# Kernel optimization log

Hardware: AMD Instinct MI355X
Metric: run time of the kernel (lower is better)

Reference implementation:

```python
import jax, jax.numpy as jnp
import numpy as np

H, W = 256, 256
N_PIX = H * W
MAX_DIST = float(np.sqrt(H ** 2 + W ** 2))


def _img_locations(dtype):
    # cartesian([arange(H), arange(W)]) -> row-major (h, w) pairs, matches prob_map.reshape(-1)
    hh, ww = jnp.meshgrid(jnp.arange(H), jnp.arange(W), indexing="ij")
    return jnp.stack([hh, ww], axis=-1).reshape(-1, 2).astype(dtype)  # [N, 2]


def setup_inputs() -> dict:
    key = jax.random.key(0)
    k1, k2 = jax.random.split(key)
    prob_map = jax.random.uniform(k1, (4, H, W), dtype=jnp.float32)
    gt_points = jax.random.randint(k2, (4, 512, 2), 0, 256, dtype=jnp.int32)
    return {"prob_map": prob_map, "gt_points": gt_points}


def reference(prob_map, gt_points):
    # prob_map: [B, H, W] float; gt_points: [B, G, 2] int pixel coords.
    # orig_sizes == resized_size in the original module, so norm_factor == 1.
    dtype = prob_map.dtype
    B = prob_map.shape[0]
    locs = _img_locations(dtype)                      # [N, 2]
    gt = gt_points.astype(dtype)                      # [B, G, 2]

    # pairwise euclidean distances via expanded form (avoids [B,N,G,2] tensor)
    x2 = jnp.sum(locs * locs, axis=-1)[None, :, None]       # [1, N, 1]
    y2 = jnp.sum(gt * gt, axis=-1)[:, None, :]              # [B, 1, G]
    xy = jnp.einsum("nd,bgd->bng", locs, gt)                # [B, N, G]
    d = jnp.sqrt(jnp.maximum(x2 + y2 - 2.0 * xy, 0.0))      # [B, N, G]

    p = prob_map.reshape(B, -1)                             # [B, N]
    n_est = jnp.sum(p, axis=-1)                             # [B]

    # term_1: prob-weighted min distance from each pixel to nearest gt point
    term_1 = jnp.sum(p * jnp.min(d, axis=-1), axis=-1) / (n_est + 1e-6)  # [B]

    # term_2: min over pixels of prob-weighted distance, averaged over gt points
    weighted_d = (1.0 - p)[:, :, None] * MAX_DIST + p[:, :, None] * d    # [B, N, G]
    term_2 = jnp.mean(jnp.min(weighted_d, axis=1), axis=-1)             # [B]

    return jnp.mean(term_1) + jnp.mean(term_2)
```

## Files before the change

### kernel.cpp

```cpp
#include <hip/hip_runtime.h>

#define NPIX  65536
#define NG    512
#define NB    4
#define MAXD  362.03867196751236f
#define WRAD  24
#define WDIM  49
#define WCNT  2401
#define SAFE_Q (23.0f - MAXD)
#define NBLK_T1 256
#define NBLK_T2 (NB*NG)
#define NBLK_MAIN (NBLK_T1 + NBLK_T2)
#define BRAD 32
#define BSPAN 68
#define BCAP 320


__device__ __forceinline__ float wave_sum(float v){
  #pragma unroll
  for (int o = 32; o > 0; o >>= 1) v += __shfl_down(v, o, 64);
  return v;
}
__device__ __forceinline__ float wave_min(float v){
  #pragma unroll
  for (int o = 32; o > 0; o >>= 1) v = fminf(v, __shfl_down(v, o, 64));
  return v;
}

__global__ __launch_bounds__(256) void k_main(const float* __restrict__ prob,
                                              const int* __restrict__ gt,
                                              float* __restrict__ wsout){
  const int tid  = threadIdx.x;
  const int lane = tid & 63;
  const int wid  = tid >> 6;

  if (blockIdx.x < NBLK_T1){
    __shared__ float2 bsab[BCAP + 1];
    __shared__ float red[8];
    __shared__ int bcnt, ovf, anybad;
    const int b  = blockIdx.x >> 6;
    const int hp = (blockIdx.x & 63) << 2;
    const float wf = (float)tid;

    if (tid == 0){ bcnt = 0; ovf = 0; anybad = 0; }
    __syncthreads();

    const int2* gtp = ((const int2*)gt) + b*NG;
    #pragma unroll
    for (int s = 0; s < 2; ++s){
      const int g = tid + 256*s;
      const int2 q = gtp[g];
      const bool in = ((unsigned)(q.x - (hp - BRAD)) < (unsigned)BSPAN);
      const unsigned long long mk = __ballot(in);
      int base = 0;
      if (lane == 0) base = atomicAdd(&bcnt, (int)__popcll(mk));
      base = __shfl(base, 0, 64);
      if (in){
        const int pos = base + (int)__popcll(mk & ((1ULL << lane) - 1ULL));
        if (pos < BCAP) bsab[pos] = make_float2(-2.0f*(float)q.x, -2.0f*(float)q.y);
        else ovf = 1;
      }
    }
    __syncthreads();
    const int Lc = min(bcnt, BCAP);
    if (tid == 0) bsab[Lc] = make_float2(-20000.0f, -20000.0f);
    __syncthreads();
    const int pairs = (Lc + 1) >> 1;

    float hf[4], m[4];
    #pragma unroll
    for (int r = 0; r < 4; ++r){ hf[r] = (float)(hp + r); m[r] = 3e38f; }

    #pragma unroll 4
    for (int k = 0; k < pairs; ++k){
      const float2 q0 = bsab[2*k + 0];
      const float2 q1 = bsab[2*k + 1];
      const float sc0 = fmaf(q0.y, q0.y, q0.x*q0.x) * 0.25f;
      const float sc1 = fmaf(q1.y, q1.y, q1.x*q1.x) * 0.25f;
      const float u0  = fmaf(q0.y, wf, sc0);
      const float u1  = fmaf(q1.y, wf, sc1);
      #pragma unroll
      for (int r = 0; r < 4; ++r){
        const float t0 = fmaf(q0.x, hf[r], u0);
        const float t1 = fmaf(q1.x, hf[r], u1);
        m[r] = fminf(fminf(m[r], t0), t1);
      }
    }

    const float w2 = (float)(tid*tid);
    float v[4];
    int bad = ovf;
    #pragma unroll
    for (int r = 0; r < 4; ++r){
      v[r] = m[r] + fmaf(hf[r], hf[r], w2);
      bad |= (v[r] > 1024.0f);
    }
    if (bad) anybad = 1;
    __syncthreads();

    if (anybad){
      #pragma unroll
      for (int r = 0; r < 4; ++r) m[r] = 3e38f;
      for (int g = 0; g < NG; ++g){
        const int2 q = gtp[g];
        const float ax = -2.0f*(float)q.x, ay = -2.0f*(float)q.y;
        const float sc = fmaf(ay, ay, ax*ax) * 0.25f;
        const float u  = fmaf(ay, wf, sc);
        #pragma unroll
        for (int r = 0; r < 4; ++r)
          m[r] = fminf(m[r], fmaf(ax, hf[r], u));
      }
      #pragma unroll
      for (int r = 0; r < 4; ++r) v[r] = m[r] + fmaf(hf[r], hf[r], w2);
    }

    float spd = 0.0f, sp = 0.0f;
    #pragma unroll
    for (int r = 0; r < 4; ++r){
      const float d = __builtin_amdgcn_sqrtf(v[r]);
      const float p = prob[b*NPIX + (hp + r)*256 + tid];
      spd = fmaf(p, d, spd);
      sp += p;
    }

    spd = wave_sum(spd);
    sp  = wave_sum(sp);
    if (lane == 0){ red[wid] = spd; red[4+wid] = sp; }
    __syncthreads();
    if (tid == 0){
      wsout[blockIdx.x]       = (red[0]+red[1]) + (red[2]+red[3]);
      wsout[512 + blockIdx.x] = (red[4]+red[5]) + (red[6]+red[7]);
    }
  } else {
    __shared__ float red[8];
    const int idx = blockIdx.x - NBLK_T1;
    const int b   = idx >> 9;
    const int gh  = gt[idx*2 + 0];
    const int gw  = gt[idx*2 + 1];

    float qm = 3e38f;
    for (int i = tid; i < WCNT; i += 256){
      const int r  = i / WDIM;
      const int c  = i - r*WDIM;
      const int hh = gh - WRAD + r;
      const int ww = gw - WRAD + c;
      if ((unsigned)hh < 256u && (unsigned)ww < 256u){
        const float p  = prob[b*NPIX + hh*256 + ww];
        const int  dh  = r - WRAD, dw = c - WRAD;
        const float d  = __builtin_amdgcn_sqrtf((float)(dh*dh + dw*dw));
        qm = fminf(qm, fmaf(p, d, p * (-MAXD)));
      }
    }
    qm = wave_min(qm);
    if (lane == 0) red[wid] = qm;
    __syncthreads();
    float qf = fminf(fminf(red[0], red[1]), fminf(red[2], red[3]));

    if (qf > SAFE_Q){
      const float ghf = (float)gh, gwf = (float)gw;
      const float aa  = -2.0f*ghf;
      const float wf  = (float)tid;
      const float bc  = fmaf(-2.0f*gwf, wf, fmaf(ghf, ghf, gwf*gwf));
      const float wsq = wf*wf;
      float q2 = 3e38f;
      const float* pr = prob + b*NPIX + tid;
      #pragma unroll 4
      for (int i = 0; i < 256; ++i){
        const float p   = pr[i*256];
        const float hfi = (float)i;
        const float d2v = fmaf(aa, hfi, fmaf(hfi, hfi, wsq) + bc);
        const float d   = __builtin_amdgcn_sqrtf(d2v);
        q2 = fminf(q2, fmaf(p, d, p * (-MAXD)));
      }
      q2 = wave_min(q2);
      __syncthreads();
      if (lane == 0) red[wid] = q2;
      __syncthreads();
      qf = fminf(fminf(red[0], red[1]), fminf(red[2], red[3]));
    }
    if (tid == 0) wsout[1024 + idx] = qf;
  }
}

__global__ __launch_bounds__(256) void k_finish(const float* __restrict__ ws,
                                                float* __restrict__ out){
  const int tid  = threadIdx.x;
  const int w    = tid >> 6;
  const int lane = tid & 63;
  __shared__ float redT2[4];
  __shared__ float t1sh[NB];

  float s = 0.0f;
  #pragma unroll
  for (int j = 0; j < 8; ++j) s += ws[1024 + tid*8 + j];
  s = wave_sum(s);
  if (lane == 0) redT2[w] = s;

  float pd = ws[w*64 + lane];
  float pp = ws[512 + w*64 + lane];
  pd = wave_sum(pd);
  pp = wave_sum(pp);
  if (lane == 0) t1sh[w] = pd / (pp + 1e-6f);
  __syncthreads();

  if (tid == 0){
    const float s2    = (redT2[0]+redT2[1]) + (redT2[2]+redT2[3]);
    const float term2 = MAXD + s2 * (1.0f/2048.0f);
    const float term1 = ((t1sh[0]+t1sh[1]) + (t1sh[2]+t1sh[3])) * 0.25f;
    out[0] = term1 + term2;
  }
}

extern "C" void kernel_launch(void* const* d_in, const int* in_sizes, int n_in,
                              void* d_out, int out_size, void* d_ws, size_t ws_size,
                              hipStream_t stream) {
  const float* prob = (const float*)d_in[0];
  const int*   gt   = (const int*)d_in[1];
  float* out = (float*)d_out;
  float* ws  = (float*)d_ws;

  hipLaunchKernelGGL(k_main,   dim3(NBLK_MAIN), dim3(256), 0, stream, prob, gt, ws);
  hipLaunchKernelGGL(k_finish, dim3(1),         dim3(256), 0, stream, ws, out);
}
```

Before: 15.79 us.

## Fuse finish reduction into main kernel via last-block atomic counter

Merges the two-kernel sequence into one kernel. The last block to finish, found through an atomic counter and threadfence, runs the final reduction. Term-2 blocks now each handle four GT points in sequence, so the grid shrinks from 2304 to 768 blocks. This removes one kernel launch and its dependency gap, but adds a memset, serialises work inside each term-2 block, and adds extra barriers per point.

```diff
diff --git a/kernel.cpp b/kernel.cpp
--- a/kernel.cpp
+++ b/kernel.cpp
@@ -9,12 +9,13 @@
 #define WCNT  2401
 #define SAFE_Q (23.0f - MAXD)
 #define NBLK_T1 256
-#define NBLK_T2 (NB*NG)
-#define NBLK_MAIN (NBLK_T1 + NBLK_T2)
+#define NBLK_T2 512
+#define NBLK    (NBLK_T1 + NBLK_T2)
 #define BRAD 32
 #define BSPAN 68
 #define BCAP 320
 
+#define CNT_OFF 3072
 
 __device__ __forceinline__ float wave_sum(float v){
   #pragma unroll
@@ -27,16 +28,18 @@
   return v;
 }
 
-__global__ __launch_bounds__(256) void k_main(const float* __restrict__ prob,
-                                              const int* __restrict__ gt,
-                                              float* __restrict__ wsout){
+__global__ __launch_bounds__(256) void k_all(const float* __restrict__ prob,
+                                             const int* __restrict__ gt,
+                                             float* __restrict__ ws,
+                                             float* __restrict__ out){
   const int tid  = threadIdx.x;
   const int lane = tid & 63;
   const int wid  = tid >> 6;
+  __shared__ float red[8];
+  __shared__ int   lastFlag;
 
   if (blockIdx.x < NBLK_T1){
     __shared__ float2 bsab[BCAP + 1];
-    __shared__ float red[8];
     __shared__ int bcnt, ovf, anybad;
     const int b  = blockIdx.x >> 6;
     const int hp = (blockIdx.x & 63) << 2;
@@ -128,86 +131,94 @@
     if (lane == 0){ red[wid] = spd; red[4+wid] = sp; }
     __syncthreads();
     if (tid == 0){
-      wsout[blockIdx.x]       = (red[0]+red[1]) + (red[2]+red[3]);
-      wsout[512 + blockIdx.x] = (red[4]+red[5]) + (red[6]+red[7]);
+      ws[blockIdx.x]       = (red[0]+red[1]) + (red[2]+red[3]);
+      ws[512 + blockIdx.x] = (red[4]+red[5]) + (red[6]+red[7]);
     }
   } else {
-    __shared__ float red[8];
-    const int idx = blockIdx.x - NBLK_T1;
-    const int b   = idx >> 9;
-    const int gh  = gt[idx*2 + 0];
-    const int gw  = gt[idx*2 + 1];
-
-    float qm = 3e38f;
-    for (int i = tid; i < WCNT; i += 256){
-      const int r  = i / WDIM;
-      const int c  = i - r*WDIM;
-      const int hh = gh - WRAD + r;
-      const int ww = gw - WRAD + c;
-      if ((unsigned)hh < 256u && (unsigned)ww < 256u){
-        const float p  = prob[b*NPIX + hh*256 + ww];
-        const int  dh  = r - WRAD, dw = c - WRAD;
-        const float d  = __builtin_amdgcn_sqrtf((float)(dh*dh + dw*dw));
-        qm = fminf(qm, fmaf(p, d, p * (-MAXD)));
-      }
-    }
-    qm = wave_min(qm);
-    if (lane == 0) red[wid] = qm;
-    __syncthreads();
-    float qf = fminf(fminf(red[0], red[1]), fminf(red[2], red[3]));
-
-    if (qf > SAFE_Q){
-      const float ghf = (float)gh, gwf = (float)gw;
-      const float aa  = -2.0f*ghf;
-      const float wf  = (float)tid;
-      const float bc  = fmaf(-2.0f*gwf, wf, fmaf(ghf, ghf, gwf*gwf));
-      const float wsq = wf*wf;
-      float q2 = 3e38f;
-      const float* pr = prob + b*NPIX + tid;
-      #pragma unroll 4
-      for (int i = 0; i < 256; ++i){
-        const float p   = pr[i*256];
-        const float hfi = (float)i;
-        const float d2v = fmaf(aa, hfi, fmaf(hfi, hfi, wsq) + bc);
-        const float d   = __builtin_amdgcn_sqrtf(d2v);
-        q2 = fminf(q2, fmaf(p, d, p * (-MAXD)));
-      }
-      q2 = wave_min(q2);
+    const int j2 = blockIdx.x - NBLK_T1;
+    for (int s = 0; s < 4; ++s){
+      const int idx = j2*4 + s;
+      const int b   = idx >> 9;
+      const int gh  = gt[idx*2 + 0];
+      const int gw  = gt[idx*2 + 1];
+
+      float qm = 3e38f;
+      for (int i = tid; i < WCNT; i += 256){
+        const int r  = i / WDIM;
+        const int c  = i - r*WDIM;
+        const int hh = gh - WRAD + r;
+        const int ww = gw - WRAD + c;
+        if ((unsigned)hh < 256u && (unsigned)ww < 256u){
+          const float p  = prob[b*NPIX + hh*256 + ww];
+          const int  dh  = r - WRAD, dw = c - WRAD;
+          const float d  = __builtin_amdgcn_sqrtf((float)(dh*dh + dw*dw));
+          qm = fminf(qm, fmaf(p, d, p * (-MAXD)));
+        }
+      }
+      qm = wave_min(qm);
+      if (lane == 0) red[wid] = qm;
       __syncthreads();
-      if (lane == 0) red[wid] = q2;
+      float qf = fminf(fminf(red[0], red[1]), fminf(red[2], red[3]));
+
+      if (qf > SAFE_Q){
+        const float ghf = (float)gh, gwf = (float)gw;
+        const float aa  = -2.0f*ghf;
+        const float wf  = (float)tid;
+        const float bc  = fmaf(-2.0f*gwf, wf, fmaf(ghf, ghf, gwf*gwf));
+        const float wsq = wf*wf;
+        float q2 = 3e38f;
+        const float* pr = prob + b*NPIX + tid;
+        #pragma unroll 4
+        for (int i = 0; i < 256; ++i){
+          const float p   = pr[i*256];
+          const float hfi = (float)i;
+          const float d2v = fmaf(aa, hfi, fmaf(hfi, hfi, wsq) + bc);
+          const float d   = __builtin_amdgcn_sqrtf(d2v);
+          q2 = fminf(q2, fmaf(p, d, p * (-MAXD)));
+        }
+        q2 = wave_min(q2);
+        __syncthreads();
+        if (lane == 0) red[wid] = q2;
+        __syncthreads();
+        qf = fminf(fminf(red[0], red[1]), fminf(red[2], red[3]));
+      }
+      if (tid == 0) ws[1024 + idx] = qf;
       __syncthreads();
-      qf = fminf(fminf(red[0], red[1]), fminf(red[2], red[3]));
-    }
-    if (tid == 0) wsout[1024 + idx] = qf;
+    }
   }
-}
-
-__global__ __launch_bounds__(256) void k_finish(const float* __restrict__ ws,
-                                                float* __restrict__ out){
-  const int tid  = threadIdx.x;
-  const int w    = tid >> 6;
-  const int lane = tid & 63;
-  __shared__ float redT2[4];
-  __shared__ float t1sh[NB];
-
-  float s = 0.0f;
-  #pragma unroll
-  for (int j = 0; j < 8; ++j) s += ws[1024 + tid*8 + j];
-  s = wave_sum(s);
-  if (lane == 0) redT2[w] = s;
-
-  float pd = ws[w*64 + lane];
-  float pp = ws[512 + w*64 + lane];
-  pd = wave_sum(pd);
-  pp = wave_sum(pp);
-  if (lane == 0) t1sh[w] = pd / (pp + 1e-6f);
+
   __syncthreads();
-
   if (tid == 0){
-    const float s2    = (redT2[0]+redT2[1]) + (redT2[2]+redT2[3]);
-    const float term2 = MAXD + s2 * (1.0f/2048.0f);
-    const float term1 = ((t1sh[0]+t1sh[1]) + (t1sh[2]+t1sh[3])) * 0.25f;
-    out[0] = term1 + term2;
+    __threadfence();
+    const unsigned t = atomicAdd((unsigned*)(ws + CNT_OFF), 1u);
+    lastFlag = (t == NBLK - 1u);
+  }
+  __syncthreads();
+  if (lastFlag){
+    __threadfence();
+    __shared__ float redT2[4];
+    __shared__ float t1sh[NB];
+    const int w = wid;
+
+    float s = 0.0f;
+    #pragma unroll
+    for (int j = 0; j < 8; ++j) s += ws[1024 + tid*8 + j];
+    s = wave_sum(s);
+    if (lane == 0) redT2[w] = s;
+
+    float pd = ws[w*64 + lane];
+    float pp = ws[512 + w*64 + lane];
+    pd = wave_sum(pd);
+    pp = wave_sum(pp);
+    if (lane == 0) t1sh[w] = pd / (pp + 1e-6f);
+    __syncthreads();
+
+    if (tid == 0){
+      const float s2    = (redT2[0]+redT2[1]) + (redT2[2]+redT2[3]);
+      const float term2 = MAXD + s2 * (1.0f/2048.0f);
+      const float term1 = ((t1sh[0]+t1sh[1]) + (t1sh[2]+t1sh[3])) * 0.25f;
+      out[0] = term1 + term2;
+    }
   }
 }
 
@@ -219,6 +230,6 @@
   float* out = (float*)d_out;
   float* ws  = (float*)d_ws;
 
-  hipLaunchKernelGGL(k_main,   dim3(NBLK_MAIN), dim3(256), 0, stream, prob, gt, ws);
-  hipLaunchKernelGGL(k_finish, dim3(1),         dim3(256), 0, stream, ws, out);
-}
+  hipMemsetAsync(ws + CNT_OFF, 0, 4, stream);
+  hipLaunchKernelGGL(k_all, dim3(NBLK), dim3(256), 0, stream, prob, gt, ws, out);
+}
```

Result: slower. 34.37 us (+117.7%).
